# Performance work log

Measured on AMD Instinct MI355X. Metric: run time of the kernel, lower is better.

## Reference

```python
import jax, jax.numpy as jnp
import numpy as np

D_MODEL = 1024
N_HEADS = 16
K_RETRIEVED = 32
BANK_SIZE = 131072
EPS = 1e-12  # matches F.normalize eps


def setup_inputs() -> dict:
    key = jax.random.key(0)
    ks = jax.random.split(key, 7)
    B, T = 8, 2048
    x = jax.random.normal(ks[0], (B, T, D_MODEL), dtype=jnp.float32)
    mem_keys = jax.random.normal(ks[1], (BANK_SIZE, D_MODEL), dtype=jnp.float32)
    mem_values = jax.random.normal(ks[2], (BANK_SIZE, D_MODEL), dtype=jnp.float32)
    s = 1.0 / np.sqrt(D_MODEL)
    Wq = jax.random.normal(ks[3], (D_MODEL, D_MODEL), dtype=jnp.float32) * s
    Wk = jax.random.normal(ks[4], (D_MODEL, D_MODEL), dtype=jnp.float32) * s
    Wv = jax.random.normal(ks[5], (D_MODEL, D_MODEL), dtype=jnp.float32) * s
    Wo = jax.random.normal(ks[6], (D_MODEL, D_MODEL), dtype=jnp.float32) * s
    gate_logit = jnp.zeros((1,), dtype=jnp.float32)
    return {"x": x, "mem_keys": mem_keys, "mem_values": mem_values,
            "Wq": Wq, "Wk": Wk, "Wv": Wv, "Wo": Wo, "gate_logit": gate_logit}


def _normalize(v):
    n = jnp.linalg.norm(v, axis=-1, keepdims=True)
    return v / jnp.maximum(n, EPS)


def reference(x, mem_keys, mem_values, Wq, Wk, Wv, Wo, gate_logit):
    B, T, D = x.shape
    H, hd, k = N_HEADS, D_MODEL // N_HEADS, K_RETRIEVED

    # --- retrieval: mean-pool query, cosine-sim top-k, gather values ---
    q = x.mean(axis=1)                       # (B, D)
    sims = _normalize(q) @ _normalize(mem_keys).T   # (B, BANK_SIZE)
    _, idx = jax.lax.top_k(sims, k)          # (B, k) descending
    retrieved = mem_values[idx]              # (B, k, d_mem)

    # --- cross-attention over retrieved docs ---
    Q = (x @ Wq).reshape(B, T, H, hd)
    K = (retrieved @ Wk).reshape(B, k, H, hd)
    V = (retrieved @ Wv).reshape(B, k, H, hd)
    scale = 1.0 / jnp.sqrt(jnp.asarray(hd, dtype=x.dtype))
    attn = jnp.einsum('bthd,bkhd->bhtk', Q, K) * scale
    attn = jax.nn.softmax(attn, axis=-1)
    ctx = jnp.einsum('bhtk,bkhd->bthd', attn, V).reshape(B, T, D)
    ctx = ctx @ Wo

    gate = jax.nn.sigmoid(gate_logit)        # (1,) broadcasts
    return x + gate * ctx
```

## Files before the change

kernel.cpp:

```cpp
#include <hip/hip_runtime.h>

#define D_MODEL 1024
#define NH 16
#define HD 64
#define KRET 32
#define BANK 131072
#define BB 8
#define TT 2048
#define MTOK 16384
#define EPSN 1e-12f

typedef __attribute__((ext_vector_type(8))) short bf16x8;
typedef __attribute__((ext_vector_type(8))) unsigned short u16x8;
typedef __attribute__((ext_vector_type(4))) float f32x4;

__device__ __forceinline__ unsigned short f2bf(float f) {
  unsigned int u = __float_as_uint(f);
  u += 0x7fffu + ((u >> 16) & 1u);
  return (unsigned short)(u >> 16);
}
__device__ __forceinline__ float bf2f(unsigned short h) {
  return __uint_as_float(((unsigned int)h) << 16);
}

__device__ __forceinline__ void gload16(const void* g, void* l) {
  __builtin_amdgcn_global_load_lds(
      (const __attribute__((address_space(1))) unsigned int*)g,
      (__attribute__((address_space(3))) unsigned int*)l, 16, 0, 0);
}

__global__ __launch_bounds__(256) void k_conv_mean(const float* __restrict__ x,
                                                   unsigned short* __restrict__ xb,
                                                   float* __restrict__ part) {
  int ch = blockIdx.x, b = blockIdx.y, tid = threadIdx.x;
  const float4* xp = (const float4*)(x + ((size_t)b * TT + ch * 32) * D_MODEL);
  ushort4* xo = (ushort4*)(xb + ((size_t)b * TT + ch * 32) * D_MODEL);
  float4 acc = {0.f, 0.f, 0.f, 0.f};
#pragma unroll 4
  for (int t = 0; t < 32; t++) {
    float4 v = xp[t * 256 + tid];
    acc.x += v.x; acc.y += v.y; acc.z += v.z; acc.w += v.w;
    ushort4 o;
    o.x = f2bf(v.x); o.y = f2bf(v.y); o.z = f2bf(v.z); o.w = f2bf(v.w);
    xo[t * 256 + tid] = o;
  }
  ((float4*)part)[((size_t)b * 64 + ch) * 256 + tid] = acc;
}

__global__ __launch_bounds__(256) void k_transW(const float* W0, const float* W1,
                                                const float* W2, const float* W3,
                                                unsigned short* T0, unsigned short* T1,
                                                unsigned short* T2, unsigned short* T3) {
  const float* W; unsigned short* T;
  switch (blockIdx.z) {
    case 0: W = W0; T = T0; break;
    case 1: W = W1; T = T1; break;
    case 2: W = W2; T = T2; break;
    default: W = W3; T = T3; break;
  }
  __shared__ float tile[64][65];
  int k0 = blockIdx.y * 64, n0 = blockIdx.x * 64;
  int tid = threadIdx.x;
#pragma unroll
  for (int i = 0; i < 16; i++) {
    int idx = tid + i * 256; int r = idx >> 6, c = idx & 63;
    tile[r][c] = W[(size_t)(k0 + r) * D_MODEL + n0 + c];
  }
  __syncthreads();
#pragma unroll
  for (int i = 0; i < 16; i++) {
    int idx = tid + i * 256; int r = idx >> 6, c = idx & 63;
    T[(size_t)(n0 + r) * D_MODEL + k0 + c] = f2bf(tile[c][r]);
  }
}

__global__ __launch_bounds__(256) void k_qnorm(const float* __restrict__ part,
                                               float* __restrict__ qn) {
  int b = blockIdx.x; int tid = threadIdx.x;
  __shared__ float red[4];
  const float4* pp = (const float4*)part + (size_t)b * 64 * 256 + tid;
  float4 a = {0.f, 0.f, 0.f, 0.f};
#pragma unroll 8
  for (int p = 0; p < 64; p++) {
    float4 v = pp[(size_t)p * 256];
    a.x += v.x; a.y += v.y; a.z += v.z; a.w += v.w;
  }
  const float sc = 1.f / (float)TT;
  a.x *= sc; a.y *= sc; a.z *= sc; a.w *= sc;
  float ss = a.x * a.x + a.y * a.y + a.z * a.z + a.w * a.w;
#pragma unroll
  for (int m = 32; m >= 1; m >>= 1) ss += __shfl_xor(ss, m);
  if ((tid & 63) == 0) red[tid >> 6] = ss;
  __syncthreads();
  float tot = red[0] + red[1] + red[2] + red[3];
  float inv = 1.f / fmaxf(sqrtf(tot), EPSN);
  float4 o = {a.x * inv, a.y * inv, a.z * inv, a.w * inv};
  ((float4*)qn)[(size_t)b * 256 + tid] = o;
}

__global__ __launch_bounds__(256) void k_sims(const float* __restrict__ mk,
                                              const float* __restrict__ qn,
                                              float* __restrict__ sims) {
  int wave = threadIdx.x >> 6, lane = threadIdx.x & 63;
  int row0 = (blockIdx.x * 4 + wave) * 4;
  float4 kv[4][4];
#pragma unroll
  for (int r = 0; r < 4; r++) {
    const float4* kr = (const float4*)(mk + (size_t)(row0 + r) * D_MODEL);
#pragma unroll
    for (int i = 0; i < 4; i++) kv[r][i] = kr[lane + 64 * i];
  }
  float ss[4] = {0.f, 0.f, 0.f, 0.f};
#pragma unroll
  for (int r = 0; r < 4; r++)
#pragma unroll
    for (int i = 0; i < 4; i++)
      ss[r] += kv[r][i].x * kv[r][i].x + kv[r][i].y * kv[r][i].y +
               kv[r][i].z * kv[r][i].z + kv[r][i].w * kv[r][i].w;
  float dots[8][4];
#pragma unroll
  for (int b = 0; b < 8; b++)
#pragma unroll
    for (int r = 0; r < 4; r++) dots[b][r] = 0.f;
#pragma unroll
  for (int b = 0; b < 8; b++) {
    const float4* qb = (const float4*)(qn + (size_t)b * D_MODEL);
#pragma unroll
    for (int i = 0; i < 4; i++) {
      float4 q4 = qb[lane + 64 * i];
#pragma unroll
      for (int r = 0; r < 4; r++)
        dots[b][r] += kv[r][i].x * q4.x + kv[r][i].y * q4.y +
                      kv[r][i].z * q4.z + kv[r][i].w * q4.w;
    }
  }
#pragma unroll
  for (int m = 32; m >= 1; m >>= 1) {
#pragma unroll
    for (int r = 0; r < 4; r++) ss[r] += __shfl_xor(ss[r], m);
#pragma unroll
    for (int b = 0; b < 8; b++)
#pragma unroll
      for (int r = 0; r < 4; r++) dots[b][r] += __shfl_xor(dots[b][r], m);
  }
  if (lane == 0) {
#pragma unroll
    for (int r = 0; r < 4; r++) {
      float inv = 1.f / fmaxf(sqrtf(ss[r]), EPSN);
#pragma unroll
      for (int b = 0; b < 8; b++)
        sims[(size_t)b * BANK + row0 + r] = dots[b][r] * inv;
    }
  }
}

__global__ __launch_bounds__(256) void k_topk_local(const float* __restrict__ sims,
                                                    float* __restrict__ cval,
                                                    int* __restrict__ cidx) {
  int b = blockIdx.y, chunk = blockIdx.x;
  int tid = threadIdx.x, wave = tid >> 6, lane = tid & 63;
  const float* sb = sims + (size_t)b * BANK + chunk * 2048;
  float v[8]; int gi[8];
#pragma unroll
  for (int j = 0; j < 8; j++) {
    int loc = j * 256 + tid;
    v[j] = sb[loc];
    gi[j] = chunk * 2048 + loc;
  }
  __shared__ float wv[4]; __shared__ int wi[4];
  __shared__ int bcast;
  for (int it = 0; it < KRET; ++it) {
    float best = -1e30f; int besti = 1 << 30;
#pragma unroll
    for (int j = 0; j < 8; j++)
      if (v[j] > best || (v[j] == best && gi[j] < besti)) { best = v[j]; besti = gi[j]; }
#pragma unroll
    for (int m = 32; m >= 1; m >>= 1) {
      float ov = __shfl_xor(best, m); int oi = __shfl_xor(besti, m);
      if (ov > best || (ov == best && oi < besti)) { best = ov; besti = oi; }
    }
    if (lane == 0) { wv[wave] = best; wi[wave] = besti; }
    __syncthreads();
    if (tid == 0) {
      float fb = wv[0]; int fi = wi[0];
      for (int w = 1; w < 4; w++)
        if (wv[w] > fb || (wv[w] == fb && wi[w] < fi)) { fb = wv[w]; fi = wi[w]; }
      bcast = fi;
      cval[((size_t)b * 64 + chunk) * KRET + it] = fb;
      cidx[((size_t)b * 64 + chunk) * KRET + it] = fi;
    }
    __syncthreads();
    int w = bcast;
#pragma unroll
    for (int j = 0; j < 8; j++)
      if (gi[j] == w) v[j] = -1e30f;
  }
}

__global__ __launch_bounds__(256) void k_topk_merge(const float* __restrict__ cval,
                                                    const int* __restrict__ cidx,
                                                    int* __restrict__ idx) {
  int b = blockIdx.x;
  int tid = threadIdx.x, wave = tid >> 6, lane = tid & 63;
  const float* cv = cval + (size_t)b * 2048;
  const int* ci = cidx + (size_t)b * 2048;
  float v[8]; int gi[8];
#pragma unroll
  for (int j = 0; j < 8; j++) {
    int loc = j * 256 + tid;
    v[j] = cv[loc];
    gi[j] = ci[loc];
  }
  __shared__ float wv[4]; __shared__ int wi[4];
  __shared__ int bcast;
  for (int it = 0; it < KRET; ++it) {
    float best = -1e30f; int besti = 1 << 30;
#pragma unroll
    for (int j = 0; j < 8; j++)
      if (v[j] > best || (v[j] == best && gi[j] < besti)) { best = v[j]; besti = gi[j]; }
#pragma unroll
    for (int m = 32; m >= 1; m >>= 1) {
      float ov = __shfl_xor(best, m); int oi = __shfl_xor(besti, m);
      if (ov > best || (ov == best && oi < besti)) { best = ov; besti = oi; }
    }
    if (lane == 0) { wv[wave] = best; wi[wave] = besti; }
    __syncthreads();
    if (tid == 0) {
      float fb = wv[0]; int fi = wi[0];
      for (int w = 1; w < 4; w++)
        if (wv[w] > fb || (wv[w] == fb && wi[w] < fi)) { fb = wv[w]; fi = wi[w]; }
      bcast = fi;
      idx[b * KRET + it] = fi;
    }
    __syncthreads();
    int w = bcast;
#pragma unroll
    for (int j = 0; j < 8; j++)
      if (gi[j] == w) v[j] = -1e30f;
  }
}

__global__ __launch_bounds__(256) void k_kvgemm(const float* __restrict__ mv,
                                                const int* __restrict__ idx_g,
                                                const unsigned short* __restrict__ Bt,
                                                float* __restrict__ Kout,
                                                float* __restrict__ Vout) {
  __shared__ __align__(16) unsigned short As[128 * 32];
  __shared__ __align__(16) unsigned short Bs[128 * 32];
  __shared__ int idxs[128];
  const int tid = threadIdx.x;
  const int wave = tid >> 6, lane = tid & 63;
  const int bm = blockIdx.x * 128, bn = blockIdx.y * 128;
  const int wm = (wave >> 1) * 64, wn = (wave & 1) * 64;
  const int frow = lane & 15, kg = lane >> 4;
  const int K = 1024;

  if (tid < 128) idxs[tid] = idx_g[bm + tid];
  __syncthreads();

  f32x4 acc[4][4] = {};

  const int row0 = tid >> 2, col0 = (tid & 3) * 8;
  const int row1 = row0 + 64;
  const int g0 = tid * 8;
  const int g1 = 2048 + tid * 8;
  const unsigned short* b0 = Bt + (size_t)(bn + (g0 >> 5)) * K + (g0 & 31);
  const unsigned short* b1 = Bt + (size_t)(bn + (g1 >> 5)) * K + (g1 & 31);
  unsigned short* lB0 = &Bs[wave * 512];
  unsigned short* lB1 = &Bs[2048 + wave * 512];
  const float* src0 = mv + (size_t)idxs[row0] * D_MODEL + col0;
  const float* src1 = mv + (size_t)idxs[row1] * D_MODEL + col0;

  for (int k0 = 0; k0 < K; k0 += 32) {
    gload16(b0 + k0, lB0);
    gload16(b1 + k0, lB1);
    float4 u0 = *(const float4*)(src0 + k0);
    float4 w0 = *(const float4*)(src0 + k0 + 4);
    float4 u1 = *(const float4*)(src1 + k0);
    float4 w1 = *(const float4*)(src1 + k0 + 4);
    u16x8 p0, p1;
    p0[0] = f2bf(u0.x); p0[1] = f2bf(u0.y); p0[2] = f2bf(u0.z); p0[3] = f2bf(u0.w);
    p0[4] = f2bf(w0.x); p0[5] = f2bf(w0.y); p0[6] = f2bf(w0.z); p0[7] = f2bf(w0.w);
    p1[0] = f2bf(u1.x); p1[1] = f2bf(u1.y); p1[2] = f2bf(u1.z); p1[3] = f2bf(u1.w);
    p1[4] = f2bf(w1.x); p1[5] = f2bf(w1.y); p1[6] = f2bf(w1.z); p1[7] = f2bf(w1.w);
    *(u16x8*)&As[row0 * 32 + col0] = p0;
    *(u16x8*)&As[row1 * 32 + col0] = p1;
    __syncthreads();
    bf16x8 fa[4], fb[4];
#pragma unroll
    for (int i = 0; i < 4; i++)
      fa[i] = *(const bf16x8*)&As[(wm + i * 16 + frow) * 32 + kg * 8];
#pragma unroll
    for (int i = 0; i < 4; i++)
      fb[i] = *(const bf16x8*)&Bs[(wn + i * 16 + frow) * 32 + kg * 8];
#pragma unroll
    for (int i = 0; i < 4; i++)
#pragma unroll
      for (int j = 0; j < 4; j++)
        acc[i][j] = __builtin_amdgcn_mfma_f32_16x16x32_bf16(fa[i], fb[j], acc[i][j], 0, 0, 0);
    __syncthreads();
  }

  const int crow = (lane >> 4) * 4, ccol = lane & 15;
#pragma unroll
  for (int i = 0; i < 4; i++)
#pragma unroll
    for (int j = 0; j < 4; j++)
#pragma unroll
      for (int r = 0; r < 4; r++) {
        int gm = bm + wm + i * 16 + crow + r;
        int gn = bn + wn + j * 16 + ccol;
        int b = gm >> 5, jj = gm & 31;
        if (gn < 1024) {
          int h = gn >> 6, d = gn & 63;
          Kout[((((size_t)b * NH + h) * KRET + jj) << 6) + d] = acc[i][j][r];
        } else {
          int gn2 = gn - 1024;
          int h = gn2 >> 6, d = gn2 & 63;
          Vout[((((size_t)b * NH + h) * KRET + jj) << 6) + d] = acc[i][j][r];
        }
      }
}

#define STG_A(SB, T)                                          \
  do {                                                        \
    const int st_ = (T) < 31 ? (T) : 31;                      \
    gload16(aS0 + st_ * 32, &ldsA[SB][ldst0]);                \
    gload16(aS1 + st_ * 32, &ldsA[SB][ldst1]);                \
  } while (0)
#define STG_B(SB, T)                                          \
  do {                                                        \
    const int st_ = (T) < 31 ? (T) : 31;                      \
    gload16(bS0 + st_ * 32, &ldsB[SB][ldst0]);                \
    gload16(bS1 + st_ * 32, &ldsB[SB][ldst1]);                \
  } while (0)
#define GPH(CB, I0, NEWB, STMT, VM)                                            \
  do {                                                                         \
    bf16x8 af[4];                                                              \
    _Pragma("unroll") for (int ii = 0; ii < 4; ii++)                           \
        af[ii] = *(const bf16x8*)&ldsA[CB][((wr * 128 + (I0 + ii) * 16 + fr) << 5) + (sA << 3)]; \
    if (NEWB) {                                                                \
      _Pragma("unroll") for (int jj = 0; jj < 4; jj++)                         \
          bf[jj] = *(const bf16x8*)&ldsB[CB][((wc * 64 + jj * 16 + fr) << 5) + (sA << 3)]; \
    }                                                                          \
    STMT;                                                                      \
    __builtin_amdgcn_s_barrier();                                              \
    __builtin_amdgcn_s_setprio(1);                                             \
    _Pragma("unroll") for (int ii = 0; ii < 4; ii++)                           \
        _Pragma("unroll") for (int jj = 0; jj < 4; jj++)                       \
            acc[I0 + ii][jj] = __builtin_amdgcn_mfma_f32_16x16x32_bf16(        \
                af[ii], bf[jj], acc[I0 + ii][jj], 0, 0, 0);                    \
    __builtin_amdgcn_s_setprio(0);                                             \
    if (VM) asm volatile("s_waitcnt vmcnt(4)" ::: "memory");                   \
    __builtin_amdgcn_s_barrier();                                              \
  } while (0)

template <int MODE>
__global__ __launch_bounds__(512, 2) void k_gemm8(const unsigned short* __restrict__ A,
                                                  const unsigned short* __restrict__ Bt,
                                                  float* __restrict__ out_f,
                                                  unsigned short* __restrict__ out_b,
                                                  const float* __restrict__ xres,
                                                  const float* __restrict__ gatep) {
  __shared__ __align__(16) unsigned short ldsA[4][8192];
  __shared__ __align__(16) unsigned short ldsB[4][8192];
  const int tid = threadIdx.x;
  const int wid = tid >> 6, lane = tid & 63;
  const int wr = wid >> 2, wc = wid & 3;
  const int fr = lane & 15, kg = lane >> 4;
  const int bm = blockIdx.x * 256, bn = blockIdx.y * 256;
  const int K = 1024;

  f32x4 acc[8][4] = {};
  bf16x8 bf[4];

  const int r0 = tid >> 2, s0 = tid & 3;
  const int sw0 = s0 ^ ((r0 >> 1) & 3);
  const int r1 = r0 + 128;
  const int sw1 = s0 ^ ((r1 >> 1) & 3);
  const unsigned short* aS0 = A + (size_t)(bm + r0) * K + sw0 * 8;
  const unsigned short* aS1 = A + (size_t)(bm + r1) * K + sw1 * 8;
  const unsigned short* bS0 = Bt + (size_t)(bn + r0) * K + sw0 * 8;
  const unsigned short* bS1 = Bt + (size_t)(bn + r1) * K + sw1 * 8;
  const int ldst0 = wid << 9;
  const int ldst1 = 4096 + (wid << 9);
  const int sA = kg ^ ((fr >> 1) & 3);

  STG_A(0, 0); STG_B(0, 0);
  STG_A(1, 1); STG_B(1, 1);
  STG_A(2, 2); STG_B(2, 2);
  asm volatile("s_waitcnt vmcnt(4)" ::: "memory");
  __builtin_amdgcn_s_barrier();

#pragma unroll 1
  for (int it = 0; it < 8; ++it) {
    const int t = it * 4;
    GPH(0, 0, 1, STG_A(3, t + 3), 0);
    GPH(0, 4, 0, STG_B(3, t + 3), 0);
    GPH(1, 0, 1, STG_A(0, t + 4), 0);
    GPH(1, 4, 0, STG_B(0, t + 4), 1);
    GPH(2, 0, 1, STG_A(1, t + 5), 0);
    GPH(2, 4, 0, STG_B(1, t + 5), 0);
    GPH(3, 0, 1, STG_A(2, t + 6), 0);
    GPH(3, 4, 0, STG_B(2, t + 6), 1);
  }

  const int crow = (lane >> 4) * 4, ccol = lane & 15;
  if (MODE == 2) {
    float gate = 1.f / (1.f + __expf(-gatep[0]));
#pragma unroll
    for (int i = 0; i < 8; i++)
#pragma unroll
      for (int j = 0; j < 4; j++)
#pragma unroll
        for (int r = 0; r < 4; r++) {
          int gm = bm + wr * 128 + i * 16 + crow + r;
          int gn = bn + wc * 64 + j * 16 + ccol;
          size_t off = (size_t)gm * D_MODEL + gn;
          out_f[off] = xres[off] + gate * acc[i][j][r];
        }
  } else {
#pragma unroll
    for (int i = 0; i < 8; i++)
#pragma unroll
      for (int j = 0; j < 4; j++)
#pragma unroll
        for (int r = 0; r < 4; r++) {
          int gm = bm + wr * 128 + i * 16 + crow + r;
          int gn = bn + wc * 64 + j * 16 + ccol;
          int b = gm >> 11, tt = gm & 2047, h = gn >> 6, d = gn & 63;
          out_b[((((size_t)b * NH + h) * TT + tt) << 6) + d] = f2bf(acc[i][j][r]);
        }
  }
}

__global__ __launch_bounds__(256) void k_attn(const unsigned short* __restrict__ Qb,
                                              const float* __restrict__ Kws,
                                              const float* __restrict__ Vws,
                                              unsigned short* __restrict__ ctx) {
  __shared__ __align__(16) unsigned short Kl[32 * 72];
  __shared__ __align__(16) unsigned short Vt[64 * 40];
  __shared__ __align__(16) unsigned short Pl[4][16 * 40];
  const int bh = blockIdx.y, b = bh >> 4, h = bh & 15;
  const int tid = threadIdx.x, wave = tid >> 6, lane = tid & 63;
  const int t0b = blockIdx.x * 256;
  {
    int doc = tid >> 3, d0 = (tid & 7) * 8;
    const float4* kp = (const float4*)(Kws + ((size_t)bh * KRET + doc) * HD + d0);
    float4 k0 = kp[0], k1 = kp[1];
    u16x8 kb;
    kb[0] = f2bf(k0.x); kb[1] = f2bf(k0.y); kb[2] = f2bf(k0.z); kb[3] = f2bf(k0.w);
    kb[4] = f2bf(k1.x); kb[5] = f2bf(k1.y); kb[6] = f2bf(k1.z); kb[7] = f2bf(k1.w);
    *(u16x8*)&Kl[doc * 72 + d0] = kb;
    const float4* vp = (const float4*)(Vws + ((size_t)bh * KRET + doc) * HD + d0);
    float4 v0 = vp[0], v1 = vp[1];
    float vv[8] = {v0.x, v0.y, v0.z, v0.w, v1.x, v1.y, v1.z, v1.w};
#pragma unroll
    for (int j = 0; j < 8; j++) Vt[(d0 + j) * 40 + doc] = f2bf(vv[j]);
  }
  __syncthreads();

  const int fr = lane & 15, kg = lane >> 4;
  const bf16x8 kb00 = *(const bf16x8*)&Kl[fr * 72 + kg * 8];
  const bf16x8 kb01 = *(const bf16x8*)&Kl[fr * 72 + 32 + kg * 8];
  const bf16x8 kb10 = *(const bf16x8*)&Kl[(16 + fr) * 72 + kg * 8];
  const bf16x8 kb11 = *(const bf16x8*)&Kl[(16 + fr) * 72 + 32 + kg * 8];
  bf16x8 vbf[4];
#pragma unroll
  for (int dt = 0; dt < 4; dt++)
    vbf[dt] = *(const bf16x8*)&Vt[(dt * 16 + fr) * 40 + kg * 8];
  unsigned short* pw = &Pl[wave][0];

#pragma unroll
  for (int sub = 0; sub < 4; ++sub) {
    const int t0 = t0b + wave * 64 + sub * 16;
    const unsigned short* qrow = Qb + ((size_t)bh * TT + t0 + fr) * HD + kg * 8;
    bf16x8 qa0 = *(const bf16x8*)(qrow);
    bf16x8 qa1 = *(const bf16x8*)(qrow + 32);
    f32x4 s0 = {}, s1 = {};
    s0 = __builtin_amdgcn_mfma_f32_16x16x32_bf16(qa0, kb00, s0, 0, 0, 0);
    s0 = __builtin_amdgcn_mfma_f32_16x16x32_bf16(qa1, kb01, s0, 0, 0, 0);
    s1 = __builtin_amdgcn_mfma_f32_16x16x32_bf16(qa0, kb10, s1, 0, 0, 0);
    s1 = __builtin_amdgcn_mfma_f32_16x16x32_bf16(qa1, kb11, s1, 0, 0, 0);
    float a0[4], a1[4], mr[4], e0[4], e1[4], sr[4];
#pragma unroll
    for (int r = 0; r < 4; r++) {
      a0[r] = s0[r] * 0.125f; a1[r] = s1[r] * 0.125f;
      mr[r] = fmaxf(a0[r], a1[r]);
    }
#pragma unroll
    for (int m = 1; m < 16; m <<= 1)
#pragma unroll
      for (int r = 0; r < 4; r++) mr[r] = fmaxf(mr[r], __shfl_xor(mr[r], m));
#pragma unroll
    for (int r = 0; r < 4; r++) {
      e0[r] = __expf(a0[r] - mr[r]); e1[r] = __expf(a1[r] - mr[r]);
      sr[r] = e0[r] + e1[r];
    }
#pragma unroll
    for (int m = 1; m < 16; m <<= 1)
#pragma unroll
      for (int r = 0; r < 4; r++) sr[r] += __shfl_xor(sr[r], m);
#pragma unroll
    for (int r = 0; r < 4; r++) {
      float inv = 1.f / sr[r];
      int tl = (lane >> 4) * 4 + r;
      pw[tl * 40 + fr] = f2bf(e0[r] * inv);
      pw[tl * 40 + 16 + fr] = f2bf(e1[r] * inv);
    }
    asm volatile("s_waitcnt lgkmcnt(0)" ::: "memory");
    bf16x8 pa = *(const bf16x8*)&pw[fr * 40 + kg * 8];
    f32x4 c[4];
#pragma unroll
    for (int dt = 0; dt < 4; dt++) {
      f32x4 z = {};
      c[dt] = __builtin_amdgcn_mfma_f32_16x16x32_bf16(pa, vbf[dt], z, 0, 0, 0);
    }
#pragma unroll
    for (int r = 0; r < 4; r++) {
      int tl = (lane >> 4) * 4 + r;
      unsigned short* crow = ctx + ((size_t)(b * TT + t0 + tl)) * D_MODEL + h * HD;
#pragma unroll
      for (int dt = 0; dt < 4; dt++)
        crow[dt * 16 + fr] = f2bf(c[dt][r]);
    }
  }
}

extern "C" void kernel_launch(void* const* d_in, const int* in_sizes, int n_in,
                              void* d_out, int out_size, void* d_ws, size_t ws_size,
                              hipStream_t stream) {
  const float* x = (const float*)d_in[0];
  const float* mk = (const float*)d_in[1];
  const float* mv = (const float*)d_in[2];
  const float* Wq = (const float*)d_in[3];
  const float* Wk = (const float*)d_in[4];
  const float* Wv = (const float*)d_in[5];
  const float* Wo = (const float*)d_in[6];
  const float* gatep = (const float*)d_in[7];
  float* out = (float*)d_out;

  char* ws = (char*)d_ws;
  unsigned short* xb   = (unsigned short*)(ws);
  unsigned short* Qb   = (unsigned short*)(ws + 33554432);
  unsigned short* WqT  = (unsigned short*)(ws + 67108864);
  unsigned short* WkvT = (unsigned short*)(ws + 69206016);
  unsigned short* WoT  = (unsigned short*)(ws + 73400320);
  float* qn    = (float*)(ws + 75497472);
  float* sims  = (float*)(ws + 75530240);
  float* part  = (float*)(ws + 75530240);
  int*   idx   = (int*)(ws + 79724544);
  float* cval  = (float*)(ws + 79725568);
  int*   cidxb = (int*)(ws + 79791104);
  float* Kws   = (float*)(ws + 79856640);
  float* Vws   = (float*)(ws + 80905216);

  k_conv_mean<<<dim3(64, 8), 256, 0, stream>>>(x, xb, part);
  k_transW<<<dim3(16, 16, 4), 256, 0, stream>>>(Wq, Wk, Wv, Wo,
                                                WqT, WkvT, WkvT + 1048576, WoT);
  k_qnorm<<<dim3(8), 256, 0, stream>>>(part, qn);
  k_sims<<<dim3(BANK / 16), 256, 0, stream>>>(mk, qn, sims);
  k_topk_local<<<dim3(64, 8), 256, 0, stream>>>(sims, cval, cidxb);
  k_topk_merge<<<dim3(8), 256, 0, stream>>>(cval, cidxb, idx);
  k_kvgemm<<<dim3(2, 16), 256, 0, stream>>>(mv, idx, WkvT, Kws, Vws);
  k_gemm8<0><<<dim3(64, 4), 512, 0, stream>>>(xb, WqT, nullptr, Qb, nullptr, nullptr);
  k_attn<<<dim3(8, 128), 256, 0, stream>>>(Qb, Kws, Vws, xb);
  k_gemm8<2><<<dim3(64, 4), 512, 0, stream>>>(xb, WoT, out, nullptr, x, gatep);
}
```

Before: 423.6 us.

## Fuse Q projection GEMM with attention and merge prep kernels

The Q projection GEMM now runs attention in its epilogue. The 256x256 tile in registers is converted to bf16 through LDS and multiplied against the per-head K and V, which are staged in the reused LDS buffer. This avoids writing the bf16 Q tensor to global memory, reading it back, and one kernel launch. The conversion/mean kernel and the weight-transpose kernel are also merged into a single launch. Costs are extra LDS traffic and added register pressure in the GEMM kernel, and attention now runs with only 256 blocks.

```diff
diff --git a/kernel.cpp b/kernel.cpp
--- a/kernel.cpp
+++ b/kernel.cpp
@@ -29,48 +29,51 @@
       (__attribute__((address_space(3))) unsigned int*)l, 16, 0, 0);
 }
 
-__global__ __launch_bounds__(256) void k_conv_mean(const float* __restrict__ x,
-                                                   unsigned short* __restrict__ xb,
-                                                   float* __restrict__ part) {
-  int ch = blockIdx.x, b = blockIdx.y, tid = threadIdx.x;
-  const float4* xp = (const float4*)(x + ((size_t)b * TT + ch * 32) * D_MODEL);
-  ushort4* xo = (ushort4*)(xb + ((size_t)b * TT + ch * 32) * D_MODEL);
-  float4 acc = {0.f, 0.f, 0.f, 0.f};
+__global__ __launch_bounds__(256) void k_prep(const float* __restrict__ x,
+                                              unsigned short* __restrict__ xb,
+                                              float* __restrict__ part,
+                                              const float* W0, const float* W1,
+                                              const float* W2, const float* W3,
+                                              unsigned short* T0, unsigned short* T1,
+                                              unsigned short* T2, unsigned short* T3) {
+  __shared__ float tile[64][65];
+  int id = blockIdx.x, tid = threadIdx.x;
+  if (id < 512) {
+    int ch = id & 63, b = id >> 6;
+    const float4* xp = (const float4*)(x + ((size_t)b * TT + ch * 32) * D_MODEL);
+    ushort4* xo = (ushort4*)(xb + ((size_t)b * TT + ch * 32) * D_MODEL);
+    float4 acc = {0.f, 0.f, 0.f, 0.f};
 #pragma unroll 4
-  for (int t = 0; t < 32; t++) {
-    float4 v = xp[t * 256 + tid];
-    acc.x += v.x; acc.y += v.y; acc.z += v.z; acc.w += v.w;
-    ushort4 o;
-    o.x = f2bf(v.x); o.y = f2bf(v.y); o.z = f2bf(v.z); o.w = f2bf(v.w);
-    xo[t * 256 + tid] = o;
-  }
-  ((float4*)part)[((size_t)b * 64 + ch) * 256 + tid] = acc;
-}
-
-__global__ __launch_bounds__(256) void k_transW(const float* W0, const float* W1,
-                                                const float* W2, const float* W3,
-                                                unsigned short* T0, unsigned short* T1,
-                                                unsigned short* T2, unsigned short* T3) {
-  const float* W; unsigned short* T;
-  switch (blockIdx.z) {
-    case 0: W = W0; T = T0; break;
-    case 1: W = W1; T = T1; break;
-    case 2: W = W2; T = T2; break;
-    default: W = W3; T = T3; break;
-  }
-  __shared__ float tile[64][65];
-  int k0 = blockIdx.y * 64, n0 = blockIdx.x * 64;
-  int tid = threadIdx.x;
-#pragma unroll
-  for (int i = 0; i < 16; i++) {
-    int idx = tid + i * 256; int r = idx >> 6, c = idx & 63;
-    tile[r][c] = W[(size_t)(k0 + r) * D_MODEL + n0 + c];
-  }
-  __syncthreads();
-#pragma unroll
-  for (int i = 0; i < 16; i++) {
-    int idx = tid + i * 256; int r = idx >> 6, c = idx & 63;
-    T[(size_t)(n0 + r) * D_MODEL + k0 + c] = f2bf(tile[c][r]);
+    for (int t = 0; t < 32; t++) {
+      float4 v = xp[t * 256 + tid];
+      acc.x += v.x; acc.y += v.y; acc.z += v.z; acc.w += v.w;
+      ushort4 o;
+      o.x = f2bf(v.x); o.y = f2bf(v.y); o.z = f2bf(v.z); o.w = f2bf(v.w);
+      xo[t * 256 + tid] = o;
+    }
+    ((float4*)part)[((size_t)b * 64 + ch) * 256 + tid] = acc;
+  } else {
+    int wid = id - 512;
+    int nx = wid & 15, ny = (wid >> 4) & 15, nz = wid >> 8;
+    const float* W; unsigned short* T;
+    switch (nz) {
+      case 0: W = W0; T = T0; break;
+      case 1: W = W1; T = T1; break;
+      case 2: W = W2; T = T2; break;
+      default: W = W3; T = T3; break;
+    }
+    int k0 = ny * 64, n0 = nx * 64;
+#pragma unroll
+    for (int i = 0; i < 16; i++) {
+      int idx = tid + i * 256; int r = idx >> 6, c = idx & 63;
+      tile[r][c] = W[(size_t)(k0 + r) * D_MODEL + n0 + c];
+    }
+    __syncthreads();
+#pragma unroll
+    for (int i = 0; i < 16; i++) {
+      int idx = tid + i * 256; int r = idx >> 6, c = idx & 63;
+      T[(size_t)(n0 + r) * D_MODEL + k0 + c] = f2bf(tile[c][r]);
+    }
   }
 }
 
@@ -322,26 +325,28 @@
       }
 }
 
-#define STG_A(SB, T)                                          \
-  do {                                                        \
-    const int st_ = (T) < 31 ? (T) : 31;                      \
-    gload16(aS0 + st_ * 32, &ldsA[SB][ldst0]);                \
-    gload16(aS1 + st_ * 32, &ldsA[SB][ldst1]);                \
+#define LDSA(SB) (LDS + (SB) * 8192)
+#define LDSB(SB) (LDS + 32768 + (SB) * 8192)
+#define STG_A(SB, T)                                  \
+  do {                                                \
+    const int st_ = (T) < 31 ? (T) : 31;              \
+    gload16(aS0 + st_ * 32, LDSA(SB) + ldst0);        \
+    gload16(aS1 + st_ * 32, LDSA(SB) + ldst1);        \
   } while (0)
-#define STG_B(SB, T)                                          \
-  do {                                                        \
-    const int st_ = (T) < 31 ? (T) : 31;                      \
-    gload16(bS0 + st_ * 32, &ldsB[SB][ldst0]);                \
-    gload16(bS1 + st_ * 32, &ldsB[SB][ldst1]);                \
+#define STG_B(SB, T)                                  \
+  do {                                                \
+    const int st_ = (T) < 31 ? (T) : 31;              \
+    gload16(bS0 + st_ * 32, LDSB(SB) + ldst0);        \
+    gload16(bS1 + st_ * 32, LDSB(SB) + ldst1);        \
   } while (0)
 #define GPH(CB, I0, NEWB, STMT, VM)                                            \
   do {                                                                         \
     bf16x8 af[4];                                                              \
     _Pragma("unroll") for (int ii = 0; ii < 4; ii++)                           \
-        af[ii] = *(const bf16x8*)&ldsA[CB][((wr * 128 + (I0 + ii) * 16 + fr) << 5) + (sA << 3)]; \
+        af[ii] = *(const bf16x8*)(LDSA(CB) + ((wr * 128 + (I0 + ii) * 16 + fr) << 5) + (sA << 3)); \
     if (NEWB) {                                                                \
       _Pragma("unroll") for (int jj = 0; jj < 4; jj++)                         \
-          bf[jj] = *(const bf16x8*)&ldsB[CB][((wc * 64 + jj * 16 + fr) << 5) + (sA << 3)]; \
+          bf[jj] = *(const bf16x8*)(LDSB(CB) + ((wc * 64 + jj * 16 + fr) << 5) + (sA << 3)); \
     }                                                                          \
     STMT;                                                                      \
     __builtin_amdgcn_s_barrier();                                              \
@@ -354,129 +359,105 @@
     if (VM) asm volatile("s_waitcnt vmcnt(4)" ::: "memory");                   \
     __builtin_amdgcn_s_barrier();                                              \
   } while (0)
-
-template <int MODE>
-__global__ __launch_bounds__(512, 2) void k_gemm8(const unsigned short* __restrict__ A,
+#define GEMM_KLOOP(Ap, Bp)                                                      \
+  const int r0 = tid >> 2, s0 = tid & 3;                                        \
+  const int sw0 = s0 ^ ((r0 >> 1) & 3);                                         \
+  const int r1 = r0 + 128;                                                      \
+  const int sw1 = s0 ^ ((r1 >> 1) & 3);                                         \
+  const unsigned short* aS0 = (Ap) + (size_t)(bm + r0) * 1024 + sw0 * 8;        \
+  const unsigned short* aS1 = (Ap) + (size_t)(bm + r1) * 1024 + sw1 * 8;        \
+  const unsigned short* bS0 = (Bp) + (size_t)(bn + r0) * 1024 + sw0 * 8;        \
+  const unsigned short* bS1 = (Bp) + (size_t)(bn + r1) * 1024 + sw1 * 8;        \
+  const int ldst0 = wid << 9;                                                   \
+  const int ldst1 = 4096 + (wid << 9);                                          \
+  const int sA = kg ^ ((fr >> 1) & 3);                                          \
+  STG_A(0, 0); STG_B(0, 0);                                                     \
+  STG_A(1, 1); STG_B(1, 1);                                                     \
+  STG_A(2, 2); STG_B(2, 2);                                                     \
+  asm volatile("s_waitcnt vmcnt(4)" ::: "memory");                              \
+  __builtin_amdgcn_s_barrier();                                                 \
+  _Pragma("unroll 1") for (int it = 0; it < 8; ++it) {                          \
+    const int t = it * 4;                                                       \
+    GPH(0, 0, 1, STG_A(3, t + 3), 0);                                           \
+    GPH(0, 4, 0, STG_B(3, t + 3), 0);                                           \
+    GPH(1, 0, 1, STG_A(0, t + 4), 0);                                           \
+    GPH(1, 4, 0, STG_B(0, t + 4), 1);                                           \
+    GPH(2, 0, 1, STG_A(1, t + 5), 0);                                           \
+    GPH(2, 4, 0, STG_B(1, t + 5), 0);                                           \
+    GPH(3, 0, 1, STG_A(2, t + 6), 0);                                           \
+    GPH(3, 4, 0, STG_B(2, t + 6), 1);                                           \
+  }
+
+__global__ __launch_bounds__(512, 2) void k_qattn(const unsigned short* __restrict__ A,
                                                   const unsigned short* __restrict__ Bt,
-                                                  float* __restrict__ out_f,
-                                                  unsigned short* __restrict__ out_b,
-                                                  const float* __restrict__ xres,
-                                                  const float* __restrict__ gatep) {
-  __shared__ __align__(16) unsigned short ldsA[4][8192];
-  __shared__ __align__(16) unsigned short ldsB[4][8192];
+                                                  const float* __restrict__ Kws,
+                                                  const float* __restrict__ Vws,
+                                                  unsigned short* __restrict__ ctx) {
+  __shared__ __align__(16) unsigned short LDS[65536];
   const int tid = threadIdx.x;
   const int wid = tid >> 6, lane = tid & 63;
   const int wr = wid >> 2, wc = wid & 3;
   const int fr = lane & 15, kg = lane >> 4;
   const int bm = blockIdx.x * 256, bn = blockIdx.y * 256;
-  const int K = 1024;
 
   f32x4 acc[8][4] = {};
   bf16x8 bf[4];
 
-  const int r0 = tid >> 2, s0 = tid & 3;
-  const int sw0 = s0 ^ ((r0 >> 1) & 3);
-  const int r1 = r0 + 128;
-  const int sw1 = s0 ^ ((r1 >> 1) & 3);
-  const unsigned short* aS0 = A + (size_t)(bm + r0) * K + sw0 * 8;
-  const unsigned short* aS1 = A + (size_t)(bm + r1) * K + sw1 * 8;
-  const unsigned short* bS0 = Bt + (size_t)(bn + r0) * K + sw0 * 8;
-  const unsigned short* bS1 = Bt + (size_t)(bn + r1) * K + sw1 * 8;
-  const int ldst0 = wid << 9;
-  const int ldst1 = 4096 + (wid << 9);
-  const int sA = kg ^ ((fr >> 1) & 3);
-
-  STG_A(0, 0); STG_B(0, 0);
-  STG_A(1, 1); STG_B(1, 1);
-  STG_A(2, 2); STG_B(2, 2);
-  asm volatile("s_waitcnt vmcnt(4)" ::: "memory");
-  __builtin_amdgcn_s_barrier();
+  GEMM_KLOOP(A, Bt)
+
+  asm volatile("s_waitcnt vmcnt(0)" ::: "memory");
+  __syncthreads();
+
+  unsigned short* Kl = LDS;
+  unsigned short* Vt = LDS + 9216;
+  unsigned short* Qs = LDS + 19456;
+  unsigned short* Pl = LDS + 28672;
+  const int b = bm >> 11;
+  const int hbase = blockIdx.y * 4;
+  {
+    int hq = tid >> 7, rem = tid & 127, doc = rem >> 2, dq = (rem & 3) * 16;
+    const float4* kp = (const float4*)(Kws + ((((size_t)b * NH + hbase + hq) * KRET + doc) << 6) + dq);
+    float4 k0 = kp[0], k1 = kp[1], k2 = kp[2], k3 = kp[3];
+    u16x8 ka, kb2;
+    ka[0] = f2bf(k0.x); ka[1] = f2bf(k0.y); ka[2] = f2bf(k0.z); ka[3] = f2bf(k0.w);
+    ka[4] = f2bf(k1.x); ka[5] = f2bf(k1.y); ka[6] = f2bf(k1.z); ka[7] = f2bf(k1.w);
+    kb2[0] = f2bf(k2.x); kb2[1] = f2bf(k2.y); kb2[2] = f2bf(k2.z); kb2[3] = f2bf(k2.w);
+    kb2[4] = f2bf(k3.x); kb2[5] = f2bf(k3.y); kb2[6] = f2bf(k3.z); kb2[7] = f2bf(k3.w);
+    *(u16x8*)&Kl[hq * 2304 + doc * 72 + dq] = ka;
+    *(u16x8*)&Kl[hq * 2304 + doc * 72 + dq + 8] = kb2;
+    const float4* vp = (const float4*)(Vws + ((((size_t)b * NH + hbase + hq) * KRET + doc) << 6) + dq);
+    float4 v0 = vp[0], v1 = vp[1], v2 = vp[2], v3 = vp[3];
+    float vv[16] = {v0.x, v0.y, v0.z, v0.w, v1.x, v1.y, v1.z, v1.w,
+                    v2.x, v2.y, v2.z, v2.w, v3.x, v3.y, v3.z, v3.w};
+#pragma unroll
+    for (int j = 0; j < 16; j++) Vt[hq * 2560 + (dq + j) * 40 + doc] = f2bf(vv[j]);
+  }
+  __syncthreads();
+
+  unsigned short* Klh = Kl + wc * 2304;
+  unsigned short* Vth = Vt + wc * 2560;
+  const bf16x8 kb00 = *(const bf16x8*)&Klh[fr * 72 + kg * 8];
+  const bf16x8 kb01 = *(const bf16x8*)&Klh[fr * 72 + 32 + kg * 8];
+  const bf16x8 kb10 = *(const bf16x8*)&Klh[(16 + fr) * 72 + kg * 8];
+  const bf16x8 kb11 = *(const bf16x8*)&Klh[(16 + fr) * 72 + 32 + kg * 8];
+  bf16x8 vbf[4];
+#pragma unroll
+  for (int dt = 0; dt < 4; dt++)
+    vbf[dt] = *(const bf16x8*)&Vth[(dt * 16 + fr) * 40 + kg * 8];
+  unsigned short* Qw = Qs + wid * 1152;
+  unsigned short* pw = Pl + wid * 640;
+  const int h = hbase + wc;
 
 #pragma unroll 1
-  for (int it = 0; it < 8; ++it) {
-    const int t = it * 4;
-    GPH(0, 0, 1, STG_A(3, t + 3), 0);
-    GPH(0, 4, 0, STG_B(3, t + 3), 0);
-    GPH(1, 0, 1, STG_A(0, t + 4), 0);
-    GPH(1, 4, 0, STG_B(0, t + 4), 1);
-    GPH(2, 0, 1, STG_A(1, t + 5), 0);
-    GPH(2, 4, 0, STG_B(1, t + 5), 0);
-    GPH(3, 0, 1, STG_A(2, t + 6), 0);
-    GPH(3, 4, 0, STG_B(2, t + 6), 1);
-  }
-
-  const int crow = (lane >> 4) * 4, ccol = lane & 15;
-  if (MODE == 2) {
-    float gate = 1.f / (1.f + __expf(-gatep[0]));
-#pragma unroll
-    for (int i = 0; i < 8; i++)
-#pragma unroll
-      for (int j = 0; j < 4; j++)
-#pragma unroll
-        for (int r = 0; r < 4; r++) {
-          int gm = bm + wr * 128 + i * 16 + crow + r;
-          int gn = bn + wc * 64 + j * 16 + ccol;
-          size_t off = (size_t)gm * D_MODEL + gn;
-          out_f[off] = xres[off] + gate * acc[i][j][r];
-        }
-  } else {
-#pragma unroll
-    for (int i = 0; i < 8; i++)
-#pragma unroll
-      for (int j = 0; j < 4; j++)
-#pragma unroll
-        for (int r = 0; r < 4; r++) {
-          int gm = bm + wr * 128 + i * 16 + crow + r;
-          int gn = bn + wc * 64 + j * 16 + ccol;
-          int b = gm >> 11, tt = gm & 2047, h = gn >> 6, d = gn & 63;
-          out_b[((((size_t)b * NH + h) * TT + tt) << 6) + d] = f2bf(acc[i][j][r]);
-        }
-  }
-}
-
-__global__ __launch_bounds__(256) void k_attn(const unsigned short* __restrict__ Qb,
-                                              const float* __restrict__ Kws,
-                                              const float* __restrict__ Vws,
-                                              unsigned short* __restrict__ ctx) {
-  __shared__ __align__(16) unsigned short Kl[32 * 72];
-  __shared__ __align__(16) unsigned short Vt[64 * 40];
-  __shared__ __align__(16) unsigned short Pl[4][16 * 40];
-  const int bh = blockIdx.y, b = bh >> 4, h = bh & 15;
-  const int tid = threadIdx.x, wave = tid >> 6, lane = tid & 63;
-  const int t0b = blockIdx.x * 256;
-  {
-    int doc = tid >> 3, d0 = (tid & 7) * 8;
-    const float4* kp = (const float4*)(Kws + ((size_t)bh * KRET + doc) * HD + d0);
-    float4 k0 = kp[0], k1 = kp[1];
-    u16x8 kb;
-    kb[0] = f2bf(k0.x); kb[1] = f2bf(k0.y); kb[2] = f2bf(k0.z); kb[3] = f2bf(k0.w);
-    kb[4] = f2bf(k1.x); kb[5] = f2bf(k1.y); kb[6] = f2bf(k1.z); kb[7] = f2bf(k1.w);
-    *(u16x8*)&Kl[doc * 72 + d0] = kb;
-    const float4* vp = (const float4*)(Vws + ((size_t)bh * KRET + doc) * HD + d0);
-    float4 v0 = vp[0], v1 = vp[1];
-    float vv[8] = {v0.x, v0.y, v0.z, v0.w, v1.x, v1.y, v1.z, v1.w};
-#pragma unroll
-    for (int j = 0; j < 8; j++) Vt[(d0 + j) * 40 + doc] = f2bf(vv[j]);
-  }
-  __syncthreads();
-
-  const int fr = lane & 15, kg = lane >> 4;
-  const bf16x8 kb00 = *(const bf16x8*)&Kl[fr * 72 + kg * 8];
-  const bf16x8 kb01 = *(const bf16x8*)&Kl[fr * 72 + 32 + kg * 8];
-  const bf16x8 kb10 = *(const bf16x8*)&Kl[(16 + fr) * 72 + kg * 8];
-  const bf16x8 kb11 = *(const bf16x8*)&Kl[(16 + fr) * 72 + 32 + kg * 8];
-  bf16x8 vbf[4];
-#pragma unroll
-  for (int dt = 0; dt < 4; dt++)
-    vbf[dt] = *(const bf16x8*)&Vt[(dt * 16 + fr) * 40 + kg * 8];
-  unsigned short* pw = &Pl[wave][0];
-
-#pragma unroll
-  for (int sub = 0; sub < 4; ++sub) {
-    const int t0 = t0b + wave * 64 + sub * 16;
-    const unsigned short* qrow = Qb + ((size_t)bh * TT + t0 + fr) * HD + kg * 8;
-    bf16x8 qa0 = *(const bf16x8*)(qrow);
-    bf16x8 qa1 = *(const bf16x8*)(qrow + 32);
+  for (int i = 0; i < 8; ++i) {
+#pragma unroll
+    for (int j = 0; j < 4; j++)
+#pragma unroll
+      for (int r = 0; r < 4; r++)
+        Qw[(kg * 4 + r) * 72 + j * 16 + fr] = f2bf(acc[i][j][r]);
+    asm volatile("s_waitcnt lgkmcnt(0)" ::: "memory");
+    bf16x8 qa0 = *(const bf16x8*)&Qw[fr * 72 + kg * 8];
+    bf16x8 qa1 = *(const bf16x8*)&Qw[fr * 72 + 32 + kg * 8];
     f32x4 s0 = {}, s1 = {};
     s0 = __builtin_amdgcn_mfma_f32_16x16x32_bf16(qa0, kb00, s0, 0, 0, 0);
     s0 = __builtin_amdgcn_mfma_f32_16x16x32_bf16(qa1, kb01, s0, 0, 0, 0);
@@ -504,7 +485,7 @@
 #pragma unroll
     for (int r = 0; r < 4; r++) {
       float inv = 1.f / sr[r];
-      int tl = (lane >> 4) * 4 + r;
+      int tl = kg * 4 + r;
       pw[tl * 40 + fr] = f2bf(e0[r] * inv);
       pw[tl * 40 + 16 + fr] = f2bf(e1[r] * inv);
     }
@@ -518,13 +499,45 @@
     }
 #pragma unroll
     for (int r = 0; r < 4; r++) {
-      int tl = (lane >> 4) * 4 + r;
-      unsigned short* crow = ctx + ((size_t)(b * TT + t0 + tl)) * D_MODEL + h * HD;
+      int tl = kg * 4 + r;
+      unsigned short* crow = ctx + ((size_t)(bm + wr * 128 + i * 16 + tl)) * D_MODEL + h * HD;
 #pragma unroll
       for (int dt = 0; dt < 4; dt++)
         crow[dt * 16 + fr] = f2bf(c[dt][r]);
     }
   }
+}
+
+__global__ __launch_bounds__(512, 2) void k_gemmO(const unsigned short* __restrict__ A,
+                                                  const unsigned short* __restrict__ Bt,
+                                                  float* __restrict__ out_f,
+                                                  const float* __restrict__ xres,
+                                                  const float* __restrict__ gatep) {
+  __shared__ __align__(16) unsigned short LDS[65536];
+  const int tid = threadIdx.x;
+  const int wid = tid >> 6, lane = tid & 63;
+  const int wr = wid >> 2, wc = wid & 3;
+  const int fr = lane & 15, kg = lane >> 4;
+  const int bm = blockIdx.x * 256, bn = blockIdx.y * 256;
+
+  f32x4 acc[8][4] = {};
+  bf16x8 bf[4];
+
+  GEMM_KLOOP(A, Bt)
+
+  const int crow = kg * 4, ccol = fr;
+  float gate = 1.f / (1.f + __expf(-gatep[0]));
+#pragma unroll
+  for (int i = 0; i < 8; i++)
+#pragma unroll
+    for (int j = 0; j < 4; j++)
+#pragma unroll
+      for (int r = 0; r < 4; r++) {
+        int gm = bm + wr * 128 + i * 16 + crow + r;
+        int gn = bn + wc * 64 + j * 16 + ccol;
+        size_t off = (size_t)gm * D_MODEL + gn;
+        out_f[off] = xres[off] + gate * acc[i][j][r];
+      }
 }
 
 extern "C" void kernel_launch(void* const* d_in, const int* in_sizes, int n_in,
@@ -542,7 +555,7 @@
 
   char* ws = (char*)d_ws;
   unsigned short* xb   = (unsigned short*)(ws);
-  unsigned short* Qb   = (unsigned short*)(ws + 33554432);
+  unsigned short* ctxb = (unsigned short*)(ws + 33554432);
   unsigned short* WqT  = (unsigned short*)(ws + 67108864);
   unsigned short* WkvT = (unsigned short*)(ws + 69206016);
   unsigned short* WoT  = (unsigned short*)(ws + 73400320);
@@ -555,15 +568,13 @@
   float* Kws   = (float*)(ws + 79856640);
   float* Vws   = (float*)(ws + 80905216);
 
-  k_conv_mean<<<dim3(64, 8), 256, 0, stream>>>(x, xb, part);
-  k_transW<<<dim3(16, 16, 4), 256, 0, stream>>>(Wq, Wk, Wv, Wo,
-                                                WqT, WkvT, WkvT + 1048576, WoT);
+  k_prep<<<dim3(1536), 256, 0, stream>>>(x, xb, part, Wq, Wk, Wv, Wo,
+                                         WqT, WkvT, WkvT + 1048576, WoT);
   k_qnorm<<<dim3(8), 256, 0, stream>>>(part, qn);
   k_sims<<<dim3(BANK / 16), 256, 0, stream>>>(mk, qn, sims);
   k_topk_local<<<dim3(64, 8), 256, 0, stream>>>(sims, cval, cidxb);
   k_topk_merge<<<dim3(8), 256, 0, stream>>>(cval, cidxb, idx);
   k_kvgemm<<<dim3(2, 16), 256, 0, stream>>>(mv, idx, WkvT, Kws, Vws);
-  k_gemm8<0><<<dim3(64, 4), 512, 0, stream>>>(xb, WqT, nullptr, Qb, nullptr, nullptr);
-  k_attn<<<dim3(8, 128), 256, 0, stream>>>(Qb, Kws, Vws, xb);
-  k_gemm8<2><<<dim3(64, 4), 512, 0, stream>>>(xb, WoT, out, nullptr, x, gatep);
-}
+  k_qattn<<<dim3(64, 4), 512, 0, stream>>>(xb, WqT, Kws, Vws, ctxb);
+  k_gemmO<<<dim3(64, 4), 512, 0, stream>>>(ctxb, WoT, out, x, gatep);
+}
```

Result: slower. 1.024 ms (+141.7%).
